# Performance work log

Measured on AMD Instinct MI355X. Metric: run time of the kernel, lower is better.

Reference implementation:

```python
import jax, jax.numpy as jnp
import numpy as np

NUM_EDGE_TYPES = 8
NUM_NODE_TYPES = 3


def _rgcn_conv(x, edge_index, edge_type, node_type, rel_W, root_W, root_b):
    """One RGCNConv layer: per-relation mean aggregation + per-node-type root transform.
    x: [N, din]; rel_W: [R, din, dout]; root_W: [T, din, dout]; root_b: [T, dout]."""
    src, dst = edge_index[0], edge_index[1]
    N = x.shape[0]
    dout = rel_W.shape[-1]
    xs = x[src]  # [E, din] gather once, reused by all relations
    out = jnp.zeros((N, dout), dtype=x.dtype)
    for r in range(rel_W.shape[0]):
        w = (edge_type == r).astype(x.dtype)  # [E] relation mask
        msg = (xs @ rel_W[r]) * w[:, None]    # [E, dout]
        s = jax.ops.segment_sum(msg, dst, num_segments=N)   # [N, dout]
        cnt = jax.ops.segment_sum(w, dst, num_segments=N)   # [N]
        out = out + jnp.where(cnt[:, None] > 0, s / jnp.maximum(cnt, 1.0)[:, None], 0.0)
    for t in range(root_W.shape[0]):
        m = (node_type == t).astype(x.dtype)[:, None]
        out = out + m * (x @ root_W[t] + root_b[t])
    return out


def _group_input(x0, x1, emb2, node_type, local_node_idx):
    # h[n] = x_{node_type[n]}[local_node_idx[n]]
    g0 = x0[local_node_idx]
    g1 = x1[local_node_idx]
    g2 = emb2[local_node_idx]
    nt = node_type[:, None]
    return jnp.where(nt == 0, g0, jnp.where(nt == 1, g1, g2))


def setup_inputs() -> dict:
    key = jax.random.key(0)
    ks = jax.random.split(key, 16)
    N_PER_TYPE, D_IN, D_H, D_OUT = 40000, 128, 128, 349
    N = 3 * N_PER_TYPE
    E = 1920000
    s_in = 1.0 / np.sqrt(D_IN)
    inp = {
        "x0": jax.random.normal(ks[0], (N_PER_TYPE, D_IN), jnp.float32),
        "x1": jax.random.normal(ks[1], (N_PER_TYPE, D_IN), jnp.float32),
        "emb2": jax.random.normal(ks[2], (N_PER_TYPE, D_IN), jnp.float32),
        "rel_W1": jax.random.normal(ks[3], (NUM_EDGE_TYPES, D_IN, D_H), jnp.float32) * s_in,
        "root_W1": jax.random.normal(ks[4], (NUM_NODE_TYPES, D_IN, D_H), jnp.float32) * s_in,
        "root_b1": jax.random.normal(ks[5], (NUM_NODE_TYPES, D_H), jnp.float32) * 0.01,
        "rel_W2": jax.random.normal(ks[6], (NUM_EDGE_TYPES, D_H, D_OUT), jnp.float32) * s_in,
        "root_W2": jax.random.normal(ks[7], (NUM_NODE_TYPES, D_H, D_OUT), jnp.float32) * s_in,
        "root_b2": jax.random.normal(ks[8], (NUM_NODE_TYPES, D_OUT), jnp.float32) * 0.01,
        "edge_index": jax.random.randint(ks[9], (2, E), 0, N, jnp.int64),
        "edge_type": jax.random.randint(ks[10], (E,), 0, NUM_EDGE_TYPES, jnp.int64),
        "node_type": jax.random.randint(ks[11], (N,), 0, NUM_NODE_TYPES, jnp.int64),
        "local_node_idx": jax.random.randint(ks[12], (N,), 0, N_PER_TYPE, jnp.int64),
    }
    return inp


def reference(x0, x1, emb2, rel_W1, root_W1, root_b1, rel_W2, root_W2, root_b2,
              edge_index, edge_type, node_type, local_node_idx):
    x = _group_input(x0, x1, emb2, node_type, local_node_idx)          # [N, D_IN]
    x = _rgcn_conv(x, edge_index, edge_type, node_type, rel_W1, root_W1, root_b1)
    x = jax.nn.relu(x)  # dropout is identity in eval mode
    x = _rgcn_conv(x, edge_index, edge_type, node_type, rel_W2, root_W2, root_b2)
    return jax.nn.log_softmax(x, axis=-1)
```

## Files before the change

### kernel.cpp

```cpp
#include <hip/hip_runtime.h>

#define DH 128
#define KTOT 1408
#define DOUT2 349
#define DOUT2P 384

typedef short v8s __attribute__((ext_vector_type(8)));
typedef float v4f __attribute__((ext_vector_type(4)));

__device__ __forceinline__ unsigned short f2bf(float f) {
  unsigned int u = __float_as_uint(f);
  u += 0x7fffu + ((u >> 16) & 1u);
  return (unsigned short)(u >> 16);
}
__device__ __forceinline__ unsigned int pack2(float a, float b) {
  return (unsigned int)f2bf(a) | ((unsigned int)f2bf(b) << 16);
}

__device__ __forceinline__ void gl2lds16(const unsigned short* g, unsigned short* l) {
  __builtin_amdgcn_global_load_lds((const __attribute__((address_space(1))) unsigned int*)g,
                                   (__attribute__((address_space(3))) unsigned int*)l, 16, 0, 0);
}

__global__ void k_detect(const int* __restrict__ nt_raw, int* __restrict__ flag, int half) {
  int i = blockIdx.x * 256 + threadIdx.x;
  if (i >= half) return;
  if (nt_raw[2 * i + 1] != 0) atomicOr(flag, 1);
}
__global__ void k_cvt(const int* __restrict__ in, int* __restrict__ out, int n,
                      const int* __restrict__ flag) {
  int i = blockIdx.x * 256 + threadIdx.x;
  if (i >= n) return;
  out[i] = (*flag) ? in[i] : in[2 * i];
}

__global__ void k_gather(const float4* __restrict__ x0, const float4* __restrict__ x1,
                         const float4* __restrict__ x2, const int* __restrict__ nt,
                         const int* __restrict__ li, ushort4* __restrict__ xout, int total) {
  int i = blockIdx.x * 256 + threadIdx.x;
  if (i >= total) return;
  int node = i >> 5, c = i & 31;
  int t = nt[node];
  int l = li[node];
  const float4* s = (t == 0) ? x0 : (t == 1) ? x1 : x2;
  float4 v = s[(size_t)l * 32 + c];
  ushort4 o;
  o.x = f2bf(v.x); o.y = f2bf(v.y); o.z = f2bf(v.z); o.w = f2bf(v.w);
  xout[i] = o;
}

__global__ void k_count(const int* __restrict__ src_dst, const int* __restrict__ et,
                        int* __restrict__ cnt, int E) {
  int i = blockIdx.x * 256 + threadIdx.x;
  if (i >= E) return;
  int dst = src_dst[E + i];
  int r = et[i];
  atomicAdd(&cnt[dst * 8 + r], 1);
}

__global__ __launch_bounds__(1024) void k_scan1(const int* __restrict__ cnt,
                                                int* __restrict__ outl,
                                                int* __restrict__ bsums, int n) {
  __shared__ int s[1024];
  int tid = threadIdx.x;
  int gid = blockIdx.x * 1024 + tid;
  int v = (gid < n) ? cnt[gid] : 0;
  s[tid] = v;
  __syncthreads();
  for (int o = 1; o < 1024; o <<= 1) {
    int t = (tid >= o) ? s[tid - o] : 0;
    __syncthreads();
    s[tid] += t;
    __syncthreads();
  }
  if (gid < n) outl[gid] = s[tid] - v;
  if (tid == 1023) bsums[blockIdx.x] = s[1023];
}
__global__ __launch_bounds__(1024) void k_scan2(int* __restrict__ bsums, int nb) {
  __shared__ int s[1024];
  int tid = threadIdx.x;
  int v = (tid < nb) ? bsums[tid] : 0;
  s[tid] = v;
  __syncthreads();
  for (int o = 1; o < 1024; o <<= 1) {
    int t = (tid >= o) ? s[tid - o] : 0;
    __syncthreads();
    s[tid] += t;
    __syncthreads();
  }
  if (tid < nb) bsums[tid] = s[tid] - v;
}
__global__ __launch_bounds__(1024) void k_scan3(int* __restrict__ offs,
                                                const int* __restrict__ bsums, int n, int total) {
  int gid = blockIdx.x * 1024 + threadIdx.x;
  if (gid < n) offs[gid] += bsums[blockIdx.x];
  if (gid == 0) offs[n] = total;
}

__global__ void k_scatter(const int* __restrict__ src_dst, const int* __restrict__ et,
                          int* __restrict__ cur, int* __restrict__ srcs, int E) {
  int i = blockIdx.x * 256 + threadIdx.x;
  if (i >= E) return;
  int dst = src_dst[E + i];
  int r = et[i];
  int pos = atomicAdd(&cur[dst * 8 + r], 1);
  srcs[pos] = src_dst[i];
}

__global__ void k_prepw(const float* __restrict__ rel,
                        const float* __restrict__ root,
                        unsigned short* __restrict__ Wt, int dout, int doutp) {
  int i = blockIdx.x * 256 + threadIdx.x;
  int tot = doutp * KTOT;
  if (i >= tot) return;
  int n = i / KTOT;
  int k = i - n * KTOT;
  unsigned short v = 0;
  if (n < dout)
    v = f2bf((k < 1024) ? rel[(size_t)k * dout + n] : root[(size_t)(k - 1024) * dout + n]);
  Wt[i] = v;
}

__global__ __launch_bounds__(256) void k_aggregate(const unsigned int* __restrict__ xin,
                                                   unsigned int* __restrict__ yout,
                                                   const int* __restrict__ offs,
                                                   const int* __restrict__ srcs,
                                                   const int* __restrict__ node_type,
                                                   int m0, int mc) {
  int wid = blockIdx.x * 4 + (threadIdx.x >> 6);
  int wl = wid >> 1;
  int h = wid & 1;
  if (wl >= mc) return;
  int w = m0 + wl;
  int lane = threadIdx.x & 63;
  unsigned int* yrow = yout + (size_t)wl * 704;
  int base = w * 8 + h * 4;
#pragma unroll
  for (int r = 0; r < 4; ++r) {
    int s = offs[base + r], e = offs[base + r + 1];
    float a0 = 0.f, a1 = 0.f, b0 = 0.f, b1 = 0.f;
    int j = s;
    for (; j + 2 <= e; j += 2) {
      int s1 = srcs[j], s2 = srcs[j + 1];
      unsigned int u1 = xin[(size_t)s1 * 64 + lane];
      unsigned int u2 = xin[(size_t)s2 * 64 + lane];
      a0 += __uint_as_float(u1 << 16);
      a1 += __uint_as_float(u1 & 0xffff0000u);
      b0 += __uint_as_float(u2 << 16);
      b1 += __uint_as_float(u2 & 0xffff0000u);
    }
    if (j < e) {
      int s1 = srcs[j];
      unsigned int u1 = xin[(size_t)s1 * 64 + lane];
      a0 += __uint_as_float(u1 << 16);
      a1 += __uint_as_float(u1 & 0xffff0000u);
    }
    int c = e - s;
    float sc = (c > 0) ? 1.0f / (float)c : 0.0f;
    yrow[(h * 4 + r) * 64 + lane] = pack2((a0 + b0) * sc, (a1 + b1) * sc);
  }
  if (h == 0) {
    unsigned int uself = xin[(size_t)w * 64 + lane];
    int nt = node_type[w];
#pragma unroll
    for (int t = 0; t < 3; ++t) yrow[(8 + t) * 64 + lane] = (nt == t) ? uself : 0u;
  }
}

__global__ __launch_bounds__(256) void k_gemm(const unsigned short* __restrict__ Y,
                                              const unsigned short* __restrict__ Wt,
                                              const int* __restrict__ node_type,
                                              const float* __restrict__ bias,
                                              unsigned short* __restrict__ outH,
                                              float* __restrict__ outF,
                                              int M, int dout, int mode) {
  __shared__ unsigned short Al[128 * 32];
  __shared__ unsigned short Bl[128 * 32];
  int tid = threadIdx.x;
  int n0 = blockIdx.x * 128;
  int m0 = blockIdx.y * 128;
  int lane = tid & 63;
  int w = tid >> 6;
  int wm = (w >> 1) * 64, wn = (w & 1) * 64;
  int l15 = lane & 15, q = lane >> 4;

  v4f acc[4][4];
#pragma unroll
  for (int i = 0; i < 4; ++i)
#pragma unroll
    for (int j = 0; j < 4; ++j) acc[i][j] = (v4f){0.f, 0.f, 0.f, 0.f};

  int rbase = 16 * (2 * w);
  const unsigned short* Ag0 = Y + (size_t)(m0 + rbase + (lane >> 2)) * KTOT + 8 * (lane & 3);
  const unsigned short* Bg0 = Wt + (size_t)(n0 + rbase + (lane >> 2)) * KTOT + 8 * (lane & 3);
  unsigned short* Asl0 = Al + (2 * w) * 512;
  unsigned short* Bsl0 = Bl + (2 * w) * 512;

  for (int k0 = 0; k0 < KTOT; k0 += 32) {
    gl2lds16(Ag0 + k0, Asl0);
    gl2lds16(Ag0 + (size_t)16 * KTOT + k0, Asl0 + 512);
    gl2lds16(Bg0 + k0, Bsl0);
    gl2lds16(Bg0 + (size_t)16 * KTOT + k0, Bsl0 + 512);
    __syncthreads();
    v8s a[4], b[4];
#pragma unroll
    for (int ti = 0; ti < 4; ++ti)
      a[ti] = *(const v8s*)(Al + (wm + ti * 16 + l15) * 32 + q * 8);
#pragma unroll
    for (int tj = 0; tj < 4; ++tj)
      b[tj] = *(const v8s*)(Bl + (wn + tj * 16 + l15) * 32 + q * 8);
#pragma unroll
    for (int ti = 0; ti < 4; ++ti)
#pragma unroll
      for (int tj = 0; tj < 4; ++tj)
        acc[ti][tj] = __builtin_amdgcn_mfma_f32_16x16x32_bf16(a[ti], b[tj], acc[ti][tj], 0, 0, 0);
    __syncthreads();
  }

#pragma unroll
  for (int ti = 0; ti < 4; ++ti) {
#pragma unroll
    for (int i = 0; i < 4; ++i) {
      int row = m0 + wm + ti * 16 + q * 4 + i;
      if (row >= M) continue;
      int nt = node_type[row];
      const float* brow = bias + nt * dout;
#pragma unroll
      for (int tj = 0; tj < 4; ++tj) {
        int col = n0 + wn + tj * 16 + l15;
        if (col >= dout) continue;
        float v = acc[ti][tj][i] + brow[col];
        if (mode == 1) {
          v = v > 0.f ? v : 0.f;
          outH[(size_t)row * dout + col] = f2bf(v);
        } else {
          outF[(size_t)row * dout + col] = v;
        }
      }
    }
  }
}

__global__ __launch_bounds__(256) void k_softmax(float* __restrict__ X, int M) {
  int w = blockIdx.x * 4 + (threadIdx.x >> 6);
  if (w >= M) return;
  int lane = threadIdx.x & 63;
  float* row = X + (size_t)w * DOUT2;
  float v[6];
  float mx = -3.0e38f;
#pragma unroll
  for (int i = 0; i < 6; ++i) {
    int c = lane + i * 64;
    v[i] = (c < DOUT2) ? row[c] : -3.0e38f;
    mx = fmaxf(mx, v[i]);
  }
#pragma unroll
  for (int o = 32; o > 0; o >>= 1) mx = fmaxf(mx, __shfl_xor(mx, o));
  float s = 0.f;
#pragma unroll
  for (int i = 0; i < 6; ++i) {
    int c = lane + i * 64;
    if (c < DOUT2) s += __expf(v[i] - mx);
  }
#pragma unroll
  for (int o = 32; o > 0; o >>= 1) s += __shfl_xor(s, o);
  float ls = __logf(s);
#pragma unroll
  for (int i = 0; i < 6; ++i) {
    int c = lane + i * 64;
    if (c < DOUT2) row[c] = v[i] - mx - ls;
  }
}

extern "C" void kernel_launch(void* const* d_in, const int* in_sizes, int n_in,
                              void* d_out, int out_size, void* d_ws, size_t ws_size,
                              hipStream_t stream) {
  const float* x0 = (const float*)d_in[0];
  const float* x1 = (const float*)d_in[1];
  const float* emb2 = (const float*)d_in[2];
  const float* relW1 = (const float*)d_in[3];
  const float* rootW1 = (const float*)d_in[4];
  const float* rootb1 = (const float*)d_in[5];
  const float* relW2 = (const float*)d_in[6];
  const float* rootW2 = (const float*)d_in[7];
  const float* rootb2 = (const float*)d_in[8];
  const int* ei_raw = (const int*)d_in[9];
  const int* et_raw = (const int*)d_in[10];
  const int* nt_raw = (const int*)d_in[11];
  const int* li_raw = (const int*)d_in[12];

  const int E = in_sizes[10];
  const int N = in_sizes[11];
  const int NK = N * 8;

  char* p = (char*)d_ws;
  auto alloc = [&](size_t bytes) {
    char* r = p;
    p += (bytes + 255) & ~(size_t)255;
    return r;
  };
  unsigned short* xbuf = (unsigned short*)alloc((size_t)N * DH * 2);
  unsigned short* hbuf = (unsigned short*)alloc((size_t)N * DH * 2);
  unsigned short* wt1 = (unsigned short*)alloc((size_t)128 * KTOT * 2);
  unsigned short* wt2 = (unsigned short*)alloc((size_t)DOUT2P * KTOT * 2);
  int* offs = (int*)alloc((size_t)(NK + 1) * 4);
  int* cur = (int*)alloc((size_t)NK * 4);
  int* srcs = (int*)alloc((size_t)E * 4);
  int* bsums = (int*)alloc(4096);
  int* ei32 = (int*)alloc((size_t)2 * E * 4);
  int* et32 = (int*)alloc((size_t)E * 4);
  int* nt32 = (int*)alloc((size_t)N * 4);
  int* li32 = (int*)alloc((size_t)N * 4);
  int* flag = (int*)alloc(256);

  size_t used = (size_t)(p - (char*)d_ws);
  size_t avail = (ws_size > used) ? (ws_size - used) : 0;
  long long maxRows = (long long)(avail / ((size_t)KTOT * 2));
  int chunk = (int)((maxRows / 128) * 128);
  int Nceil = ((N + 127) / 128) * 128;
  if (chunk > Nceil) chunk = Nceil;
  if (chunk < 128) chunk = 128;
  unsigned short* ych = (unsigned short*)p;

  float* outF = (float*)d_out;
  const int nScanBlocks = (NK + 1023) / 1024;

  hipMemsetAsync(flag, 0, 4, stream);
  hipMemsetAsync(cur, 0, (size_t)NK * 4, stream);
  k_detect<<<(N / 2 + 255) / 256, 256, 0, stream>>>(nt_raw, flag, N / 2);
  k_cvt<<<(2 * E + 255) / 256, 256, 0, stream>>>(ei_raw, ei32, 2 * E, flag);
  k_cvt<<<(E + 255) / 256, 256, 0, stream>>>(et_raw, et32, E, flag);
  k_cvt<<<(N + 255) / 256, 256, 0, stream>>>(nt_raw, nt32, N, flag);
  k_cvt<<<(N + 255) / 256, 256, 0, stream>>>(li_raw, li32, N, flag);

  k_gather<<<(N * 32 + 255) / 256, 256, 0, stream>>>((const float4*)x0, (const float4*)x1,
                                                     (const float4*)emb2, nt32, li32,
                                                     (ushort4*)xbuf, N * 32);
  k_count<<<(E + 255) / 256, 256, 0, stream>>>(ei32, et32, cur, E);
  k_scan1<<<nScanBlocks, 1024, 0, stream>>>(cur, offs, bsums, NK);
  k_scan2<<<1, 1024, 0, stream>>>(bsums, nScanBlocks);
  k_scan3<<<nScanBlocks, 1024, 0, stream>>>(offs, bsums, NK, E);
  hipMemcpyAsync(cur, offs, (size_t)NK * 4, hipMemcpyDeviceToDevice, stream);
  k_scatter<<<(E + 255) / 256, 256, 0, stream>>>(ei32, et32, cur, srcs, E);
  k_prepw<<<(128 * KTOT + 255) / 256, 256, 0, stream>>>(relW1, rootW1, wt1, 128, 128);
  k_prepw<<<(DOUT2P * KTOT + 255) / 256, 256, 0, stream>>>(relW2, rootW2, wt2, DOUT2, DOUT2P);
  for (int m0 = 0; m0 < N; m0 += chunk) {
    int mc = (N - m0 < chunk) ? (N - m0) : chunk;
    k_aggregate<<<(2 * mc + 3) / 4, 256, 0, stream>>>((const unsigned int*)xbuf,
                                                      (unsigned int*)ych, offs, srcs, nt32, m0, mc);
    dim3 g1(1, (mc + 127) / 128);
    k_gemm<<<g1, 256, 0, stream>>>(ych, wt1, nt32 + m0, rootb1, hbuf + (size_t)m0 * DH,
                                   (float*)nullptr, mc, 128, 1);
  }
  for (int m0 = 0; m0 < N; m0 += chunk) {
    int mc = (N - m0 < chunk) ? (N - m0) : chunk;
    k_aggregate<<<(2 * mc + 3) / 4, 256, 0, stream>>>((const unsigned int*)hbuf,
                                                      (unsigned int*)ych, offs, srcs, nt32, m0, mc);
    dim3 g2(DOUT2P / 128, (mc + 127) / 128);
    k_gemm<<<g2, 256, 0, stream>>>(ych, wt2, nt32 + m0, rootb2, (unsigned short*)nullptr,
                                   outF + (size_t)m0 * DOUT2, mc, DOUT2, 2);
  }
  k_softmax<<<(N + 3) / 4, 256, 0, stream>>>(outF, N);
}
```

Baseline: 1.356 ms.

## Fuse neighbor aggregation into GEMM, building A tiles directly in LDS

Replaces the separate aggregate kernel plus chunked GEMM with one fused kernel per layer. For each 128-node tile and each relation slot, the kernel gathers and mean-reduces neighbor features straight into LDS, then multiplies that slice against the matching weight rows with MFMA. This drops the large intermediate Y buffer, which was written and read back at K=1408 per row. The trade-off is that the irregular gather now sits on the GEMM's critical path with little overlap, and layer 2 has only mtiles blocks of 512 threads.

After: 1.811 ms. 33.5% more time.

```diff
diff --git a/kernel.cpp b/kernel.cpp
--- a/kernel.cpp
+++ b/kernel.cpp
@@ -2,6 +2,7 @@
 
 #define DH 128
 #define KTOT 1408
+#define NSLOT 11
 #define DOUT2 349
 #define DOUT2P 384
 
@@ -16,7 +17,6 @@
 __device__ __forceinline__ unsigned int pack2(float a, float b) {
   return (unsigned int)f2bf(a) | ((unsigned int)f2bf(b) << 16);
 }
-
 __device__ __forceinline__ void gl2lds16(const unsigned short* g, unsigned short* l) {
   __builtin_amdgcn_global_load_lds((const __attribute__((address_space(1))) unsigned int*)g,
                                    (__attribute__((address_space(3))) unsigned int*)l, 16, 0, 0);
@@ -53,9 +53,7 @@
                         int* __restrict__ cnt, int E) {
   int i = blockIdx.x * 256 + threadIdx.x;
   if (i >= E) return;
-  int dst = src_dst[E + i];
-  int r = et[i];
-  atomicAdd(&cnt[dst * 8 + r], 1);
+  atomicAdd(&cnt[src_dst[E + i] * 8 + et[i]], 1);
 }
 
 __global__ __launch_bounds__(1024) void k_scan1(const int* __restrict__ cnt,
@@ -101,9 +99,7 @@
                           int* __restrict__ cur, int* __restrict__ srcs, int E) {
   int i = blockIdx.x * 256 + threadIdx.x;
   if (i >= E) return;
-  int dst = src_dst[E + i];
-  int r = et[i];
-  int pos = atomicAdd(&cur[dst * 8 + r], 1);
+  int pos = atomicAdd(&cur[src_dst[E + i] * 8 + et[i]], 1);
   srcs[pos] = src_dst[i];
 }
 
@@ -121,100 +117,97 @@
   Wt[i] = v;
 }
 
-__global__ __launch_bounds__(256) void k_aggregate(const unsigned int* __restrict__ xin,
-                                                   unsigned int* __restrict__ yout,
-                                                   const int* __restrict__ offs,
-                                                   const int* __restrict__ srcs,
-                                                   const int* __restrict__ node_type,
-                                                   int m0, int mc) {
-  int wid = blockIdx.x * 4 + (threadIdx.x >> 6);
-  int wl = wid >> 1;
-  int h = wid & 1;
-  if (wl >= mc) return;
-  int w = m0 + wl;
-  int lane = threadIdx.x & 63;
-  unsigned int* yrow = yout + (size_t)wl * 704;
-  int base = w * 8 + h * 4;
-#pragma unroll
-  for (int r = 0; r < 4; ++r) {
-    int s = offs[base + r], e = offs[base + r + 1];
-    float a0 = 0.f, a1 = 0.f, b0 = 0.f, b1 = 0.f;
-    int j = s;
-    for (; j + 2 <= e; j += 2) {
-      int s1 = srcs[j], s2 = srcs[j + 1];
-      unsigned int u1 = xin[(size_t)s1 * 64 + lane];
-      unsigned int u2 = xin[(size_t)s2 * 64 + lane];
-      a0 += __uint_as_float(u1 << 16);
-      a1 += __uint_as_float(u1 & 0xffff0000u);
-      b0 += __uint_as_float(u2 << 16);
-      b1 += __uint_as_float(u2 & 0xffff0000u);
+template <int NT>
+__global__ __launch_bounds__(512) void k_fused(const unsigned int* __restrict__ Xu,
+                                               const unsigned short* __restrict__ Wt,
+                                               const int* __restrict__ offs,
+                                               const int* __restrict__ srcs,
+                                               const int* __restrict__ node_type,
+                                               const float* __restrict__ bias,
+                                               unsigned short* __restrict__ outH,
+                                               float* __restrict__ outF,
+                                               int M, int dout, int relu) {
+  __shared__ unsigned short Al[4 * 128 * 32];
+  __shared__ unsigned short Bl[NT * 128 * 32];
+  unsigned int* Alu = (unsigned int*)Al;
+
+  const int tid = threadIdx.x;
+  const int lane = tid & 63;
+  const int w = tid >> 6;
+  const int l15 = lane & 15, q = lane >> 4;
+  const int wm = (w >> 2) * 64;
+  const int TN = NT * 32;
+  const int wn = (w & 3) * TN;
+  const int m0 = blockIdx.x * 128;
+
+  v4f acc[4][2 * NT];
+#pragma unroll
+  for (int i = 0; i < 4; ++i)
+#pragma unroll
+    for (int j = 0; j < 2 * NT; ++j) acc[i][j] = (v4f){0.f, 0.f, 0.f, 0.f};
+
+  const int brow = lane >> 2, bseg = lane & 3;
+
+#pragma unroll 1
+  for (int r = 0; r < NSLOT; ++r) {
+#pragma unroll 1
+    for (int t = 0; t < 16; ++t) {
+      int nd = w * 16 + t;
+      int gn = m0 + nd;
+      unsigned int val = 0u;
+      if (gn < M) {
+        if (r < 8) {
+          int s = offs[gn * 8 + r], e = offs[gn * 8 + r + 1];
+          float a0 = 0.f, a1 = 0.f, b0 = 0.f, b1 = 0.f;
+          int j = s;
+          for (; j + 2 <= e; j += 2) {
+            int s1 = srcs[j], s2 = srcs[j + 1];
+            unsigned int u1 = Xu[(size_t)s1 * 64 + lane];
+            unsigned int u2 = Xu[(size_t)s2 * 64 + lane];
+            a0 += __uint_as_float(u1 << 16);
+            a1 += __uint_as_float(u1 & 0xffff0000u);
+            b0 += __uint_as_float(u2 << 16);
+            b1 += __uint_as_float(u2 & 0xffff0000u);
+          }
+          if (j < e) {
+            unsigned int u1 = Xu[(size_t)srcs[j] * 64 + lane];
+            a0 += __uint_as_float(u1 << 16);
+            a1 += __uint_as_float(u1 & 0xffff0000u);
+          }
+          int c = e - s;
+          if (c > 0) {
+            float sc = 1.0f / (float)c;
+            val = pack2((a0 + b0) * sc, (a1 + b1) * sc);
+          }
+        } else {
+          val = (node_type[gn] == r - 8) ? Xu[(size_t)gn * 64 + lane] : 0u;
+        }
+      }
+      Alu[q * 2048 + nd * 16 + l15] = val;
     }
-    if (j < e) {
-      int s1 = srcs[j];
-      unsigned int u1 = xin[(size_t)s1 * 64 + lane];
-      a0 += __uint_as_float(u1 << 16);
-      a1 += __uint_as_float(u1 & 0xffff0000u);
+
+#pragma unroll 1
+    for (int kk = 0; kk < 4; ++kk) {
+      for (int c = w; c < NT * 8; c += 8) {
+        int R = c * 16;
+        gl2lds16(Wt + (size_t)(R + brow) * KTOT + r * 128 + kk * 32 + bseg * 8,
+                 Bl + R * 32);
+      }
+      __syncthreads();
+      v8s a[4], b[2 * NT];
+#pragma unroll
+      for (int ti = 0; ti < 4; ++ti)
+        a[ti] = *(const v8s*)(Al + kk * 4096 + (wm + ti * 16 + l15) * 32 + q * 8);
+#pragma unroll
+      for (int tj = 0; tj < 2 * NT; ++tj)
+        b[tj] = *(const v8s*)(Bl + (wn + tj * 16 + l15) * 32 + q * 8);
+#pragma unroll
+      for (int ti = 0; ti < 4; ++ti)
+#pragma unroll
+        for (int tj = 0; tj < 2 * NT; ++tj)
+          acc[ti][tj] = __builtin_amdgcn_mfma_f32_16x16x32_bf16(a[ti], b[tj], acc[ti][tj], 0, 0, 0);
+      __syncthreads();
     }
-    int c = e - s;
-    float sc = (c > 0) ? 1.0f / (float)c : 0.0f;
-    yrow[(h * 4 + r) * 64 + lane] = pack2((a0 + b0) * sc, (a1 + b1) * sc);
-  }
-  if (h == 0) {
-    unsigned int uself = xin[(size_t)w * 64 + lane];
-    int nt = node_type[w];
-#pragma unroll
-    for (int t = 0; t < 3; ++t) yrow[(8 + t) * 64 + lane] = (nt == t) ? uself : 0u;
-  }
-}
-
-__global__ __launch_bounds__(256) void k_gemm(const unsigned short* __restrict__ Y,
-                                              const unsigned short* __restrict__ Wt,
-                                              const int* __restrict__ node_type,
-                                              const float* __restrict__ bias,
-                                              unsigned short* __restrict__ outH,
-                                              float* __restrict__ outF,
-                                              int M, int dout, int mode) {
-  __shared__ unsigned short Al[128 * 32];
-  __shared__ unsigned short Bl[128 * 32];
-  int tid = threadIdx.x;
-  int n0 = blockIdx.x * 128;
-  int m0 = blockIdx.y * 128;
-  int lane = tid & 63;
-  int w = tid >> 6;
-  int wm = (w >> 1) * 64, wn = (w & 1) * 64;
-  int l15 = lane & 15, q = lane >> 4;
-
-  v4f acc[4][4];
-#pragma unroll
-  for (int i = 0; i < 4; ++i)
-#pragma unroll
-    for (int j = 0; j < 4; ++j) acc[i][j] = (v4f){0.f, 0.f, 0.f, 0.f};
-
-  int rbase = 16 * (2 * w);
-  const unsigned short* Ag0 = Y + (size_t)(m0 + rbase + (lane >> 2)) * KTOT + 8 * (lane & 3);
-  const unsigned short* Bg0 = Wt + (size_t)(n0 + rbase + (lane >> 2)) * KTOT + 8 * (lane & 3);
-  unsigned short* Asl0 = Al + (2 * w) * 512;
-  unsigned short* Bsl0 = Bl + (2 * w) * 512;
-
-  for (int k0 = 0; k0 < KTOT; k0 += 32) {
-    gl2lds16(Ag0 + k0, Asl0);
-    gl2lds16(Ag0 + (size_t)16 * KTOT + k0, Asl0 + 512);
-    gl2lds16(Bg0 + k0, Bsl0);
-    gl2lds16(Bg0 + (size_t)16 * KTOT + k0, Bsl0 + 512);
-    __syncthreads();
-    v8s a[4], b[4];
-#pragma unroll
-    for (int ti = 0; ti < 4; ++ti)
-      a[ti] = *(const v8s*)(Al + (wm + ti * 16 + l15) * 32 + q * 8);
-#pragma unroll
-    for (int tj = 0; tj < 4; ++tj)
-      b[tj] = *(const v8s*)(Bl + (wn + tj * 16 + l15) * 32 + q * 8);
-#pragma unroll
-    for (int ti = 0; ti < 4; ++ti)
-#pragma unroll
-      for (int tj = 0; tj < 4; ++tj)
-        acc[ti][tj] = __builtin_amdgcn_mfma_f32_16x16x32_bf16(a[ti], b[tj], acc[ti][tj], 0, 0, 0);
-    __syncthreads();
   }
 
 #pragma unroll
@@ -224,13 +217,13 @@
       int row = m0 + wm + ti * 16 + q * 4 + i;
       if (row >= M) continue;
       int nt = node_type[row];
-      const float* brow = bias + nt * dout;
-#pragma unroll
-      for (int tj = 0; tj < 4; ++tj) {
-        int col = n0 + wn + tj * 16 + l15;
+      const float* brw = bias + nt * dout;
+#pragma unroll
+      for (int tj = 0; tj < 2 * NT; ++tj) {
+        int col = wn + tj * 16 + l15;
         if (col >= dout) continue;
-        float v = acc[ti][tj][i] + brow[col];
-        if (mode == 1) {
+        float v = acc[ti][tj][i] + brw[col];
+        if (relu) {
           v = v > 0.f ? v : 0.f;
           outH[(size_t)row * dout + col] = f2bf(v);
         } else {
@@ -313,17 +306,9 @@
   int* li32 = (int*)alloc((size_t)N * 4);
   int* flag = (int*)alloc(256);
 
-  size_t used = (size_t)(p - (char*)d_ws);
-  size_t avail = (ws_size > used) ? (ws_size - used) : 0;
-  long long maxRows = (long long)(avail / ((size_t)KTOT * 2));
-  int chunk = (int)((maxRows / 128) * 128);
-  int Nceil = ((N + 127) / 128) * 128;
-  if (chunk > Nceil) chunk = Nceil;
-  if (chunk < 128) chunk = 128;
-  unsigned short* ych = (unsigned short*)p;
-
   float* outF = (float*)d_out;
   const int nScanBlocks = (NK + 1023) / 1024;
+  const int mtiles = (N + 127) / 128;
 
   hipMemsetAsync(flag, 0, 4, stream);
   hipMemsetAsync(cur, 0, (size_t)NK * 4, stream);
@@ -344,21 +329,9 @@
   k_scatter<<<(E + 255) / 256, 256, 0, stream>>>(ei32, et32, cur, srcs, E);
   k_prepw<<<(128 * KTOT + 255) / 256, 256, 0, stream>>>(relW1, rootW1, wt1, 128, 128);
   k_prepw<<<(DOUT2P * KTOT + 255) / 256, 256, 0, stream>>>(relW2, rootW2, wt2, DOUT2, DOUT2P);
-  for (int m0 = 0; m0 < N; m0 += chunk) {
-    int mc = (N - m0 < chunk) ? (N - m0) : chunk;
-    k_aggregate<<<(2 * mc + 3) / 4, 256, 0, stream>>>((const unsigned int*)xbuf,
-                                                      (unsigned int*)ych, offs, srcs, nt32, m0, mc);
-    dim3 g1(1, (mc + 127) / 128);
-    k_gemm<<<g1, 256, 0, stream>>>(ych, wt1, nt32 + m0, rootb1, hbuf + (size_t)m0 * DH,
-                                   (float*)nullptr, mc, 128, 1);
-  }
-  for (int m0 = 0; m0 < N; m0 += chunk) {
-    int mc = (N - m0 < chunk) ? (N - m0) : chunk;
-    k_aggregate<<<(2 * mc + 3) / 4, 256, 0, stream>>>((const unsigned int*)hbuf,
-                                                      (unsigned int*)ych, offs, srcs, nt32, m0, mc);
-    dim3 g2(DOUT2P / 128, (mc + 127) / 128);
-    k_gemm<<<g2, 256, 0, stream>>>(ych, wt2, nt32 + m0, rootb2, (unsigned short*)nullptr,
-                                   outF + (size_t)m0 * DOUT2, mc, DOUT2, 2);
-  }
+  k_fused<1><<<mtiles, 512, 0, stream>>>((const unsigned int*)xbuf, wt1, offs, srcs, nt32,
+                                         rootb1, hbuf, (float*)nullptr, N, 128, 1);
+  k_fused<3><<<mtiles, 512, 0, stream>>>((const unsigned int*)hbuf, wt2, offs, srcs, nt32,
+                                         rootb2, (unsigned short*)nullptr, outF, N, DOUT2, 0);
   k_softmax<<<(N + 3) / 4, 256, 0, stream>>>(outF, N);
 }
```
